# Performance work log

Hardware: AMD Instinct MI355X
Metric: run time of the kernel (lower is better)

Reference implementation:

```python
import jax, jax.numpy as jnp
import numpy as np

MASK_FILL = -1e10
LOG_2PI = float(np.log(2.0 * np.pi))


def setup_inputs() -> dict:
    key = jax.random.key(0)
    k1, k2, k3 = jax.random.split(key, 3)
    bs, seq_len, emb_dim = 32, 512, 512
    T = 2048
    emb = jax.random.normal(k1, (bs, seq_len, emb_dim), dtype=jnp.float32)
    # positive durations; rescale so the max total duration over the batch == T exactly,
    # matching torch's T = sum(durations).int().max()
    d = jax.random.uniform(k2, (bs, seq_len), dtype=jnp.float32, minval=0.5, maxval=1.0)
    d = d * (T / jnp.max(jnp.sum(d, axis=1)))
    log_sigma = jax.random.normal(k3, (1,), dtype=jnp.float32) * 0.1
    return {"emb": emb, "durations": d, "log_sigma": log_sigma, "T": T}


def reference(emb, durations, log_sigma, T):
    # emb: (bs, S, E); durations: (bs, S); log_sigma: (1,); T: static int
    bs, S, E = emb.shape
    ls = log_sigma[0]
    sigma = jnp.exp(ls)
    # Gaussian centers per token: cumsum - 0.5*dur  -> (bs, S)
    centers = jnp.cumsum(durations, axis=1) - 0.5 * durations
    t = jnp.arange(T, dtype=emb.dtype)  # frame indices (T,)
    # Normal(loc=centers, scale=sigma).log_prob(t + 0.5)  -> (bs, T, S)
    z = (t[None, :, None] + 0.5 - centers[:, None, :]) / sigma
    logp = -0.5 * z * z - ls - 0.5 * LOG_2PI
    # mask out zero-duration tokens
    logp = jnp.where((durations == 0.0)[:, None, :], MASK_FILL, logp)
    w = jax.nn.softmax(logp, axis=2)  # (bs, T, S)
    x = jnp.einsum('bts,bse->bte', w, emb)  # (bs, T, E)
    total = jnp.sum(durations, axis=1)  # (bs,)
    out_mask = t[None, :] < total[:, None]  # (bs, T) bool
    return x, out_mask
```

## Files before the change

### kernel.cpp

```cpp
#include <hip/hip_runtime.h>
#include <math.h>

#define BS 32
#define S_TOK 512
#define E_DIM 512
#define T_FR 2048
#define FPB 8
#define WMAX 64
#define THRESH -88.0f


typedef float vfloat4 __attribute__((ext_vector_type(4)));

struct RowMeta { float m; float inv_l; int lo; int cnt; };

__global__ __launch_bounds__(64) void scan_kernel(
    const float* __restrict__ dur,
    float* __restrict__ centers,
    float* __restrict__ totals) {
  int b = blockIdx.x;
  int lane = threadIdx.x;
  const float* d = dur + b * S_TOK;
  int base = lane * 8;
  double local[8];
  double run = 0.0;
#pragma unroll
  for (int i = 0; i < 8; ++i) { run += (double)d[base + i]; local[i] = run; }
  double sum = run;
#pragma unroll
  for (int off = 1; off < 64; off <<= 1) {
    double v = __shfl_up(sum, off, 64);
    if (lane >= off) sum += v;
  }
  double excl = sum - run;
#pragma unroll
  for (int i = 0; i < 8; ++i) {
    centers[b * S_TOK + base + i] =
        (float)(excl + local[i] - 0.5 * (double)d[base + i]);
  }
  if (lane == 63) totals[b] = (float)sum;
}

__global__ __launch_bounds__(256) void meta_kernel(
    const float* __restrict__ centers,
    const float* __restrict__ log_sigma,
    RowMeta* __restrict__ meta) {
  int b = blockIdx.x >> 3;
  int t = ((blockIdx.x & 7) << 8) + threadIdx.x;

  __shared__ float cbS[S_TOK];
  for (int i = threadIdx.x; i < S_TOK; i += 256)
    cbS[i] = centers[b * S_TOK + i];
  __syncthreads();

  float inv_sigma = expf(-log_sigma[0]);
  float tq = (float)t + 0.5f;

  auto V = [&](int s) {
    float z = (tq - cbS[s]) * inv_sigma;
    return -0.5f * z * z;
  };

  int lo = 0, hi = S_TOK;
  while (lo < hi) {
    int mid = (lo + hi) >> 1;
    if (cbS[mid] < tq) lo = mid + 1; else hi = mid;
  }
  int best; float m;
  if (lo == 0) { best = 0; m = V(0); }
  else if (lo == S_TOK) { best = S_TOK - 1; m = V(best); }
  else {
    float va = V(lo - 1), vb = V(lo);
    if (va >= vb) { best = lo - 1; m = va; } else { best = lo; m = vb; }
  }

  int wl = best, wh = best;
  while (wl > 0 && V(wl - 1) > m + THRESH) --wl;
  while (wh < S_TOK - 1 && V(wh + 1) > m + THRESH) ++wh;

  float l = 0.0f;
  for (int s = wl; s <= wh; ++s) l += expf(V(s) - m);

  RowMeta mt;
  mt.m = m;
  mt.inv_l = 1.0f / l;
  mt.lo = wl;
  mt.cnt = wh - wl + 1;
  meta[b * T_FR + t] = mt;
}

__global__ __launch_bounds__(128) void fused_kernel(
    const float* __restrict__ emb,
    const float* __restrict__ centers,
    const float* __restrict__ log_sigma,
    const RowMeta* __restrict__ meta,
    const float* __restrict__ totals,
    float* __restrict__ x,
    float* __restrict__ mask_out) {
  int id = blockIdx.x;
  int sw = ((id & 7) << 10) + (id >> 3);
  int b = sw >> 8;
  int t0 = (sw & 255) << 3;

  int tid = threadIdx.x;

  __shared__ float wT[WMAX][FPB];
  __shared__ RowMeta metaS[FPB];

  if (tid < FPB) metaS[tid] = meta[b * T_FR + t0 + tid];
  __syncthreads();

  int ulo = metaS[0].lo, uhi = metaS[0].lo + metaS[0].cnt - 1;
#pragma unroll
  for (int f = 1; f < FPB; ++f) {
    ulo = min(ulo, metaS[f].lo);
    uhi = max(uhi, metaS[f].lo + metaS[f].cnt - 1);
  }
  int cnt = min(uhi - ulo + 1, WMAX);

  float inv_sigma = expf(-log_sigma[0]);
  const float* cb = centers + b * S_TOK;

  for (int k = tid; k < cnt * FPB; k += 128) {
    int i = k >> 3, f = k & 7;
    float c = cb[ulo + i];
    float tqf = (float)(t0 + f) + 0.5f;
    float z = (tqf - c) * inv_sigma;
    float v = -0.5f * z * z;
    wT[i][f] = expf(v - metaS[f].m) * metaS[f].inv_l;
  }
  __syncthreads();

  const vfloat4* e4 =
      (const vfloat4*)emb + ((size_t)(b * S_TOK + ulo)) * (E_DIM / 4) + tid;
  vfloat4 acc[FPB];
#pragma unroll
  for (int f = 0; f < FPB; ++f) acc[f] = (vfloat4){0.f, 0.f, 0.f, 0.f};

#pragma unroll 2
  for (int i = 0; i < cnt; ++i) {
    vfloat4 v = e4[(size_t)i * (E_DIM / 4)];
    const vfloat4* wp = (const vfloat4*)&wT[i][0];
    vfloat4 w0 = wp[0], w1 = wp[1];
    acc[0] += w0.x * v; acc[1] += w0.y * v;
    acc[2] += w0.z * v; acc[3] += w0.w * v;
    acc[4] += w1.x * v; acc[5] += w1.y * v;
    acc[6] += w1.z * v; acc[7] += w1.w * v;
  }

  vfloat4* xp = (vfloat4*)x + ((size_t)(b * T_FR + t0)) * (E_DIM / 4) + tid;
#pragma unroll
  for (int f = 0; f < FPB; ++f)
    __builtin_nontemporal_store(acc[f], xp + f * (E_DIM / 4));

  if (tid < FPB) {
    int t = t0 + tid;
    mask_out[b * T_FR + t] = ((float)t < totals[b]) ? 1.0f : 0.0f;
  }
}

extern "C" void kernel_launch(void* const* d_in, const int* in_sizes, int n_in,
                              void* d_out, int out_size, void* d_ws,
                              size_t ws_size, hipStream_t stream) {
  const float* emb = (const float*)d_in[0];
  const float* dur = (const float*)d_in[1];
  const float* log_sigma = (const float*)d_in[2];

  float* x = (float*)d_out;
  float* mask_out = x + (size_t)BS * T_FR * E_DIM;

  float* centers = (float*)d_ws;
  float* totals = centers + BS * S_TOK;
  RowMeta* meta = (RowMeta*)(totals + 64);

  scan_kernel<<<BS, 64, 0, stream>>>(dur, centers, totals);
  meta_kernel<<<BS * 8, 256, 0, stream>>>(centers, log_sigma, meta);
  fused_kernel<<<(BS * T_FR) / FPB, 128, 0, stream>>>(
      emb, centers, log_sigma, meta, totals, x, mask_out);
}
```

Before: 176.3 us.

## Process 16 frames per block with tighter softmax window and prefetched embedding rows

Doubles the frames handled per block from 8 to 16, so each embedding row loaded is reused across more output frames. It also tightens the softmax truncation threshold and cap on the token window, and zeroes weights below the threshold. The inner loop is software-pipelined so the next embedding row is fetched while the current one is accumulated. This raises register use (16 vec4 accumulators), which can cut occupancy, and the tighter threshold drops small softmax terms and changes the approximation.

```diff
diff --git a/kernel.cpp b/kernel.cpp
--- a/kernel.cpp
+++ b/kernel.cpp
@@ -5,9 +5,9 @@
 #define S_TOK 512
 #define E_DIM 512
 #define T_FR 2048
-#define FPB 8
-#define WMAX 64
-#define THRESH -88.0f
+#define FPB 16
+#define WMAX 32
+#define THRESH -25.0f
 
 
 typedef float vfloat4 __attribute__((ext_vector_type(4)));
@@ -98,9 +98,9 @@
     float* __restrict__ x,
     float* __restrict__ mask_out) {
   int id = blockIdx.x;
-  int sw = ((id & 7) << 10) + (id >> 3);
-  int b = sw >> 8;
-  int t0 = (sw & 255) << 3;
+  int sw = ((id & 7) << 9) + (id >> 3);
+  int b = sw >> 7;
+  int t0 = (sw & 127) << 4;
 
   int tid = threadIdx.x;
 
@@ -122,12 +122,13 @@
   const float* cb = centers + b * S_TOK;
 
   for (int k = tid; k < cnt * FPB; k += 128) {
-    int i = k >> 3, f = k & 7;
+    int i = k >> 4, f = k & 15;
     float c = cb[ulo + i];
     float tqf = (float)(t0 + f) + 0.5f;
     float z = (tqf - c) * inv_sigma;
     float v = -0.5f * z * z;
-    wT[i][f] = expf(v - metaS[f].m) * metaS[f].inv_l;
+    float e = expf(v - metaS[f].m) * metaS[f].inv_l;
+    wT[i][f] = (v - metaS[f].m > THRESH) ? e : 0.0f;
   }
   __syncthreads();
 
@@ -137,15 +138,32 @@
 #pragma unroll
   for (int f = 0; f < FPB; ++f) acc[f] = (vfloat4){0.f, 0.f, 0.f, 0.f};
 
-#pragma unroll 2
-  for (int i = 0; i < cnt; ++i) {
-    vfloat4 v = e4[(size_t)i * (E_DIM / 4)];
+  vfloat4 vcur = e4[0];
+  for (int i = 0; i < cnt - 1; ++i) {
+    vfloat4 vnext = e4[(size_t)(i + 1) * (E_DIM / 4)];
     const vfloat4* wp = (const vfloat4*)&wT[i][0];
-    vfloat4 w0 = wp[0], w1 = wp[1];
-    acc[0] += w0.x * v; acc[1] += w0.y * v;
-    acc[2] += w0.z * v; acc[3] += w0.w * v;
-    acc[4] += w1.x * v; acc[5] += w1.y * v;
-    acc[6] += w1.z * v; acc[7] += w1.w * v;
+    vfloat4 w0 = wp[0], w1 = wp[1], w2 = wp[2], w3 = wp[3];
+    acc[0] += w0.x * vcur;  acc[1] += w0.y * vcur;
+    acc[2] += w0.z * vcur;  acc[3] += w0.w * vcur;
+    acc[4] += w1.x * vcur;  acc[5] += w1.y * vcur;
+    acc[6] += w1.z * vcur;  acc[7] += w1.w * vcur;
+    acc[8] += w2.x * vcur;  acc[9] += w2.y * vcur;
+    acc[10] += w2.z * vcur; acc[11] += w2.w * vcur;
+    acc[12] += w3.x * vcur; acc[13] += w3.y * vcur;
+    acc[14] += w3.z * vcur; acc[15] += w3.w * vcur;
+    vcur = vnext;
+  }
+  {
+    const vfloat4* wp = (const vfloat4*)&wT[cnt - 1][0];
+    vfloat4 w0 = wp[0], w1 = wp[1], w2 = wp[2], w3 = wp[3];
+    acc[0] += w0.x * vcur;  acc[1] += w0.y * vcur;
+    acc[2] += w0.z * vcur;  acc[3] += w0.w * vcur;
+    acc[4] += w1.x * vcur;  acc[5] += w1.y * vcur;
+    acc[6] += w1.z * vcur;  acc[7] += w1.w * vcur;
+    acc[8] += w2.x * vcur;  acc[9] += w2.y * vcur;
+    acc[10] += w2.z * vcur; acc[11] += w2.w * vcur;
+    acc[12] += w3.x * vcur; acc[13] += w3.y * vcur;
+    acc[14] += w3.z * vcur; acc[15] += w3.w * vcur;
   }
 
   vfloat4* xp = (vfloat4*)x + ((size_t)(b * T_FR + t0)) * (E_DIM / 4) + tid;
```

Result: no change. 176.4 us (+0.1%).
